# Performance work log

Measured on AMD Instinct MI355X. Metric: run time of the kernel, lower is better.

## Reference

```python
import jax, jax.numpy as jnp
import numpy as np

DIM, HEADS, DIM_HEAD = 1024, 16, 64
INNER = HEADS * DIM_HEAD
EPS = 1e-5

def layernorm(x, w, b):
    mu = jnp.mean(x, axis=-1, keepdims=True)
    var = jnp.var(x, axis=-1, keepdims=True)
    return (x - mu) / jnp.sqrt(var + EPS) * w + b

def setup_inputs() -> dict:
    key = jax.random.key(0)
    ks = jax.random.split(key, 8)
    s = lambda d: 1.0 / np.sqrt(d)
    return {
        'x': jax.random.normal(ks[0], (4, 2048, DIM), jnp.float32),
        'media': jax.random.normal(ks[1], (4, 1024, DIM), jnp.float32),
        'ln_w': jnp.ones((DIM,), jnp.float32),
        'ln_b': jnp.zeros((DIM,), jnp.float32),
        'Wq': jax.random.normal(ks[2], (DIM, INNER), jnp.float32) * s(DIM),
        'Wkv': jax.random.normal(ks[3], (DIM, 2 * INNER), jnp.float32) * s(DIM),
        'Wo': jax.random.normal(ks[4], (INNER, DIM), jnp.float32) * s(INNER),
        'attn_gate': jnp.zeros((1,), jnp.float32),
        'ffln_w': jnp.ones((DIM,), jnp.float32),
        'ffln_b': jnp.zeros((DIM,), jnp.float32),
        'W1': jax.random.normal(ks[5], (DIM, 4 * DIM), jnp.float32) * s(DIM),
        'W2': jax.random.normal(ks[6], (4 * DIM, DIM), jnp.float32) * s(4 * DIM),
    }

def reference(x, media, ln_w, ln_b, Wq, Wkv, Wo, attn_gate, ffln_w, ffln_b, W1, W2):
    scale = DIM_HEAD ** (-0.5)
    b, n, _ = x.shape
    m = media.shape[1]
    # MaskedCrossAttention
    xn = layernorm(x, ln_w, ln_b)
    q = (xn @ Wq).reshape(b, n, HEADS, DIM_HEAD).transpose(0, 2, 1, 3)  # b h n d
    kv = media @ Wkv
    k, v = jnp.split(kv, 2, axis=-1)
    k = k.reshape(b, m, HEADS, DIM_HEAD).transpose(0, 2, 1, 3)  # b h m d
    v = v.reshape(b, m, HEADS, DIM_HEAD).transpose(0, 2, 1, 3)
    sim = jnp.einsum('bhid,bhjd->bhij', q * scale, k)
    # original subtracts detached row-max then softmax: identical to stable softmax
    attn = jax.nn.softmax(sim, axis=-1)
    out = jnp.einsum('bhij,bhjd->bhid', attn, v)
    out = out.transpose(0, 2, 1, 3).reshape(b, n, INNER) @ Wo
    x = out * jnp.tanh(attn_gate) + x
    # FeedForward (note: ff_gate exists in module but is unused in forward)
    h = layernorm(x, ffln_w, ffln_b) @ W1
    h = jax.nn.gelu(h, approximate=False) @ W2
    return h + x
```

## Files before the change

kernel.cpp:

```cpp
#include <hip/hip_runtime.h>
#include <hip/hip_bf16.h>

using bf16 = __hip_bfloat16;
typedef __attribute__((ext_vector_type(8))) short short8;
typedef __attribute__((ext_vector_type(4))) float f32x4;

typedef const void __attribute__((address_space(1))) gvoid;
typedef void __attribute__((address_space(3))) svoid;

__device__ __forceinline__ f32x4 mfma16(short8 a, short8 b, f32x4 c) {
    return __builtin_amdgcn_mfma_f32_16x16x32_bf16(a, b, c, 0, 0, 0);
}

__device__ __forceinline__ void async16(void* lds, const void* g) {
    __builtin_amdgcn_global_load_lds((gvoid*)g, (svoid*)lds, 16, 0, 0);
}

__device__ __forceinline__ unsigned short f2b(float f) {
    bf16 h = __float2bfloat16(f);
    unsigned short u;
    __builtin_memcpy(&u, &h, 2);
    return u;
}

__device__ __forceinline__ float fast_gelu(float x) {
    const float z0 = fmaf(x * x * x, 0.1029432f, 2.3022083f * x);
    const float z = fminf(z0, 80.0f);
    const float e = __builtin_amdgcn_exp2f(z);
    return x * e / (1.0f + e);
}

__global__ __launch_bounds__(256) void prep(
    const float* __restrict__ Wq, const float* __restrict__ Wkv,
    const float* __restrict__ Wo, const float* __restrict__ W1,
    const float* __restrict__ W2, bf16* __restrict__ WqT, bf16* __restrict__ WkvT,
    bf16* __restrict__ WoT, bf16* __restrict__ W1T, bf16* __restrict__ W2T,
    const float* __restrict__ media, bf16* __restrict__ mediab,
    const float* __restrict__ gate, float* __restrict__ gatet) {
    int id = blockIdx.x;
    const float* in;
    bf16* outp;
    int K, N, bx, by;
    if (id < 1024) {
        in = Wq; outp = WqT; K = 1024; N = 1024; bx = id & 31; by = id >> 5;
    } else if (id < 3072) {
        id -= 1024; in = Wkv; outp = WkvT; K = 1024; N = 2048; bx = id & 63; by = id >> 6;
    } else if (id < 4096) {
        id -= 3072; in = Wo; outp = WoT; K = 1024; N = 1024; bx = id & 31; by = id >> 5;
    } else if (id < 8192) {
        id -= 4096; in = W1; outp = W1T; K = 1024; N = 4096; bx = id & 127; by = id >> 7;
    } else if (id < 12288) {
        id -= 8192; in = W2; outp = W2T; K = 4096; N = 1024; bx = id & 31; by = id >> 5;
    } else {
        if (blockIdx.x == 12288 && threadIdx.x == 0) gatet[0] = tanhf(gate[0]);
        id -= 12288;
        const size_t i = (size_t)id * 256 + threadIdx.x;
        float4 v = ((const float4*)media)[i];
        ushort4 o;
        o.x = f2b(v.x); o.y = f2b(v.y); o.z = f2b(v.z); o.w = f2b(v.w);
        ((ushort4*)mediab)[i] = o;
        return;
    }
    __shared__ float tile[32][33];
    const int tx = threadIdx.x & 31, ty = threadIdx.x >> 5;
    const int n0 = bx * 32, k0 = by * 32;
#pragma unroll
    for (int j = 0; j < 32; j += 8)
        tile[ty + j][tx] = in[(size_t)(k0 + ty + j) * N + n0 + tx];
    __syncthreads();
#pragma unroll
    for (int j = 0; j < 32; j += 8)
        outp[(size_t)(n0 + ty + j) * K + k0 + tx] = __float2bfloat16(tile[tx][ty + j]);
}

__global__ __launch_bounds__(256) void layernorm_bf16(
    const float* __restrict__ x, const float* __restrict__ w,
    const float* __restrict__ b, bf16* __restrict__ out) {
    const int row = blockIdx.x, t = threadIdx.x;
    const float4 v = ((const float4*)(x + (size_t)row * 1024))[t];
    float s = v.x + v.y + v.z + v.w;
    float s2 = v.x * v.x + v.y * v.y + v.z * v.z + v.w * v.w;
#pragma unroll
    for (int off = 1; off < 64; off <<= 1) {
        s += __shfl_xor(s, off);
        s2 += __shfl_xor(s2, off);
    }
    __shared__ float rs[4], rs2[4];
    if ((t & 63) == 0) { rs[t >> 6] = s; rs2[t >> 6] = s2; }
    __syncthreads();
    const float S = rs[0] + rs[1] + rs[2] + rs[3];
    const float S2 = rs2[0] + rs2[1] + rs2[2] + rs2[3];
    const float mean = S * (1.0f / 1024.0f);
    const float var = S2 * (1.0f / 1024.0f) - mean * mean;
    const float rstd = rsqrtf(var + 1e-5f);
    const float4 wv = ((const float4*)w)[t];
    const float4 bv = ((const float4*)b)[t];
    ushort4 o;
    o.x = f2b((v.x - mean) * rstd * wv.x + bv.x);
    o.y = f2b((v.y - mean) * rstd * wv.y + bv.y);
    o.z = f2b((v.z - mean) * rstd * wv.z + bv.z);
    o.w = f2b((v.w - mean) * rstd * wv.w + bv.w);
    ((ushort4*)(out + (size_t)row * 1024))[t] = o;
}

__global__ __launch_bounds__(256) void vtranspose(
    const bf16* __restrict__ kvb, bf16* __restrict__ vtg) {
    const int mt = blockIdx.x, bh = blockIdx.y;
    const int b = bh >> 4, h = bh & 15;
    const int m0 = mt * 64;
    __shared__ bf16 tile[64 * 72];
    const int t = threadIdx.x;
#pragma unroll
    for (int i = 0; i < 2; ++i) {
        const int m = i * 32 + (t >> 3);
        short8 v = *(const short8*)(kvb + ((size_t)b * 1024 + m0 + m) * 2048 + 1024 +
                                    (size_t)h * 64 + (t & 7) * 8);
        *(short8*)&tile[m * 72 + (t & 7) * 8] = v;
    }
    __syncthreads();
#pragma unroll
    for (int i = 0; i < 2; ++i) {
        const int d = i * 32 + (t >> 3);
        const int mb = (t & 7) * 8;
        bf16 tmp[8];
#pragma unroll
        for (int j = 0; j < 8; ++j) tmp[j] = tile[(mb + j) * 72 + d];
        *(short8*)(vtg + (size_t)bh * 65536 + (size_t)d * 1024 + m0 + mb) = *(short8*)tmp;
    }
}

enum { EPI_BF16 = 0, EPI_GELU = 1, EPI_GATE_RES = 2, EPI_RES = 3 };

template <int EPI>
__global__ __launch_bounds__(256) void gemm_bf16(
    const bf16* __restrict__ A, const bf16* __restrict__ BT, void* __restrict__ Cout,
    const float* __restrict__ res, const float* __restrict__ gate_p,
    int M, int N, int K) {
    __shared__ bf16 As[2][128 * 64];
    __shared__ bf16 Bs[2][128 * 64];
    const int t = threadIdx.x;
    const int lane = t & 63;
    const int quad = lane >> 4, l15 = lane & 15;
    const int wave = t >> 6;
    const int wm = (wave >> 1) * 64, wn = (wave & 1) * 64;
    const int bm = blockIdx.x * 128, bn = blockIdx.y * 128;

    const int sr = t >> 3;
    const int sc = (t & 7) ^ (sr & 7);
    const bf16* Ag = A + (size_t)(bm + sr) * K + sc * 8;
    const bf16* Bg = BT + (size_t)(bn + sr) * K + sc * 8;

    f32x4 acc[4][4] = {};

    auto stage = [&](int buf, int k0) {
#pragma unroll
        for (int i = 0; i < 4; ++i) {
            async16(&As[buf][i * 2048 + t * 8], Ag + (size_t)i * 32 * K + k0);
            async16(&Bs[buf][i * 2048 + t * 8], Bg + (size_t)i * 32 * K + k0);
        }
    };
    auto compute = [&](int buf) {
#pragma unroll
        for (int dk = 0; dk < 2; ++dk) {
            short8 af[4], bfr[4];
#pragma unroll
            for (int i = 0; i < 4; ++i)
                af[i] = *(const short8*)&As[buf][(wm + i * 16 + l15) * 64 +
                                                 (((dk * 4 + quad) ^ (l15 & 7)) * 8)];
#pragma unroll
            for (int i = 0; i < 4; ++i)
                bfr[i] = *(const short8*)&Bs[buf][(wn + i * 16 + l15) * 64 +
                                                  (((dk * 4 + quad) ^ (l15 & 7)) * 8)];
#pragma unroll
            for (int i = 0; i < 4; ++i)
#pragma unroll
                for (int j = 0; j < 4; ++j)
                    acc[i][j] = mfma16(af[i], bfr[j], acc[i][j]);
        }
    };

    stage(0, 0);
    int cur = 0;
    for (int k0 = 64; k0 < K; k0 += 64) {
        __syncthreads();
        stage(cur ^ 1, k0);
        compute(cur);
        cur ^= 1;
    }
    __syncthreads();
    compute(cur);

    const float gate = (EPI == EPI_GATE_RES) ? gate_p[0] : 0.0f;
#pragma unroll
    for (int i = 0; i < 4; ++i) {
#pragma unroll
        for (int j = 0; j < 4; ++j) {
#pragma unroll
            for (int r = 0; r < 4; ++r) {
                const int row = bm + wm + i * 16 + quad * 4 + r;
                const int col = bn + wn + j * 16 + l15;
                const size_t idx = (size_t)row * N + col;
                const float v = acc[i][j][r];
                if constexpr (EPI == EPI_BF16) {
                    ((bf16*)Cout)[idx] = __float2bfloat16(v);
                } else if constexpr (EPI == EPI_GELU) {
                    ((bf16*)Cout)[idx] = __float2bfloat16(fast_gelu(v));
                } else if constexpr (EPI == EPI_GATE_RES) {
                    ((float*)Cout)[idx] = gate * v + res[idx];
                } else {
                    ((float*)Cout)[idx] = v + res[idx];
                }
            }
        }
    }
}

__global__ __launch_bounds__(256) void attention(
    const bf16* __restrict__ q, const bf16* __restrict__ kvb,
    const bf16* __restrict__ vtg, bf16* __restrict__ out) {
    const int bh = blockIdx.y;
    const int b = bh >> 4, h = bh & 15;
    const int t = threadIdx.x;
    const int wave = t >> 6, lane = t & 63;
    const int quad = lane >> 4, l15 = lane & 15;
    const int qrow0 = blockIdx.x * 128 + wave * 32;

    __shared__ bf16 Ks[2][128 * 64];
    __shared__ bf16 Vts[2][64 * 128];
    __shared__ bf16 Ps[4][16 * 128];

    short8 qa[2][2];
    const size_t qbase = ((size_t)b * 2048 + qrow0) * 1024 + (size_t)h * 64;
#pragma unroll
    for (int g = 0; g < 2; ++g)
#pragma unroll
        for (int dk = 0; dk < 2; ++dk)
            qa[g][dk] = *(const short8*)(q + qbase + (size_t)(g * 16 + l15) * 1024 + dk * 32 + quad * 8);

    f32x4 o[2][4] = {};
    float lsum[2][4] = {};

    const int km = t >> 3;
    const int kc = (t & 7) ^ (km & 7);
    const bf16* ksrc = kvb + ((size_t)b * 1024 + km) * 2048 + (size_t)h * 64 + kc * 8;
    const int vd = t >> 4;
    const int vc = (t & 15) ^ vd;
    const bf16* vsrc = vtg + (size_t)bh * 65536 + (size_t)vd * 1024 + vc * 8;

    bf16* Pw = &Ps[wave][0];

    auto stage = [&](int buf, int m0) {
#pragma unroll
        for (int i = 0; i < 4; ++i) {
            async16(&Ks[buf][i * 2048 + t * 8], ksrc + ((size_t)m0 + i * 32) * 2048);
            async16(&Vts[buf][i * 2048 + t * 8], vsrc + (size_t)i * 16 * 1024 + m0);
        }
    };

    stage(0, 0);
    for (int mc = 0; mc < 8; ++mc) {
        const int cur = mc & 1;
        __syncthreads();
        if (mc < 7) stage(cur ^ 1, (mc + 1) * 128);

#pragma unroll
        for (int g = 0; g < 2; ++g) {
#pragma unroll
            for (int mt = 0; mt < 8; ++mt) {
                f32x4 s = {};
#pragma unroll
                for (int dk = 0; dk < 2; ++dk) {
                    short8 kb = *(const short8*)&Ks[cur][(mt * 16 + l15) * 64 +
                                                    (((dk * 4 + quad) ^ (l15 & 7)) * 8)];
                    s = mfma16(qa[g][dk], kb, s);
                }
                const int pc = mt * 2 + (l15 >> 3);
                const int pj = l15 & 7;
#pragma unroll
                for (int r = 0; r < 4; ++r) {
                    const int row = quad * 4 + r;
                    const float p = __builtin_amdgcn_exp2f(
                        fmaf(s[r], 0.18033688f, -11.5415603f));
                    lsum[g][r] += p;
                    Pw[row * 128 + ((pc ^ row) & 15) * 8 + pj] = __float2bfloat16(p);
                }
            }
            asm volatile("s_waitcnt lgkmcnt(0)" ::: "memory");

#pragma unroll
            for (int ks = 0; ks < 4; ++ks) {
                short8 pa = *(const short8*)&Pw[l15 * 128 + (((ks * 4 + quad) ^ l15) & 15) * 8];
#pragma unroll
                for (int nt = 0; nt < 4; ++nt) {
                    short8 vb = *(const short8*)&Vts[cur][(nt * 16 + l15) * 128 +
                                                     (((ks * 4 + quad) ^ l15) & 15) * 8];
                    o[g][nt] = mfma16(pa, vb, o[g][nt]);
                }
            }
            asm volatile("s_waitcnt lgkmcnt(0)" ::: "memory");
        }
    }

#pragma unroll
    for (int g = 0; g < 2; ++g)
#pragma unroll
        for (int r = 0; r < 4; ++r) {
            float ls = lsum[g][r];
#pragma unroll
            for (int d = 1; d < 16; d <<= 1) ls += __shfl_xor(ls, d);
            lsum[g][r] = 1.0f / ls;
        }

#pragma unroll
    for (int g = 0; g < 2; ++g)
#pragma unroll
        for (int nt = 0; nt < 4; ++nt)
#pragma unroll
            for (int r = 0; r < 4; ++r)
                out[((size_t)b * 2048 + qrow0 + g * 16 + quad * 4 + r) * 1024 +
                    (size_t)h * 64 + nt * 16 + l15] =
                    __float2bfloat16(o[g][nt][r] * lsum[g][r]);
}


extern "C" void kernel_launch(void* const* d_in, const int* in_sizes, int n_in,
                              void* d_out, int out_size, void* d_ws, size_t ws_size,
                              hipStream_t stream) {
    const float* x    = (const float*)d_in[0];
    const float* media= (const float*)d_in[1];
    const float* ln_w = (const float*)d_in[2];
    const float* ln_b = (const float*)d_in[3];
    const float* Wq   = (const float*)d_in[4];
    const float* Wkv  = (const float*)d_in[5];
    const float* Wo   = (const float*)d_in[6];
    const float* gate = (const float*)d_in[7];
    const float* ffw  = (const float*)d_in[8];
    const float* ffb  = (const float*)d_in[9];
    const float* W1   = (const float*)d_in[10];
    const float* W2   = (const float*)d_in[11];
    float* out = (float*)d_out;

    char* p = (char*)d_ws;
    bf16* WqT    = (bf16*)p;               p += (size_t)1024 * 1024 * 2;
    bf16* WkvT   = (bf16*)p;               p += (size_t)2048 * 1024 * 2;
    bf16* WoT    = (bf16*)p;               p += (size_t)1024 * 1024 * 2;
    bf16* W1T    = (bf16*)p;               p += (size_t)4096 * 1024 * 2;
    bf16* W2T    = (bf16*)p;               p += (size_t)1024 * 4096 * 2;
    bf16* xn     = (bf16*)p;               p += (size_t)8192 * 1024 * 2;
    bf16* mediab = (bf16*)p;               p += (size_t)4096 * 1024 * 2;
    bf16* qb     = (bf16*)p;               p += (size_t)8192 * 1024 * 2;
    bf16* kvb    = (bf16*)p;               p += (size_t)4096 * 2048 * 2;
    bf16* vtg    = (bf16*)p;               p += (size_t)64 * 64 * 1024 * 2;
    bf16* attnb  = (bf16*)p;               p += (size_t)8192 * 1024 * 2;
    bf16* hb     = (bf16*)p;               p += (size_t)8192 * 4096 * 2;
    float* x2    = (float*)p;              p += (size_t)8192 * 1024 * 4;
    float* gatet = (float*)p;              p += 256;
    bf16* x2n = xn;

    prep<<<16384, 256, 0, stream>>>(Wq, Wkv, Wo, W1, W2, WqT, WkvT, WoT, W1T, W2T,
                                    media, mediab, gate, gatet);

    layernorm_bf16<<<8192, 256, 0, stream>>>(x, ln_w, ln_b, xn);
    gemm_bf16<EPI_BF16><<<dim3(64, 8), 256, 0, stream>>>(xn, WqT, qb, nullptr, nullptr, 8192, 1024, 1024);
    gemm_bf16<EPI_BF16><<<dim3(32, 16), 256, 0, stream>>>(mediab, WkvT, kvb, nullptr, nullptr, 4096, 2048, 1024);
    vtranspose<<<dim3(16, 64), 256, 0, stream>>>(kvb, vtg);
    attention<<<dim3(16, 64), 256, 0, stream>>>(qb, kvb, vtg, attnb);
    gemm_bf16<EPI_GATE_RES><<<dim3(64, 8), 256, 0, stream>>>(attnb, WoT, x2, x, gatet, 8192, 1024, 1024);

    layernorm_bf16<<<8192, 256, 0, stream>>>(x2, ffw, ffb, x2n);
    gemm_bf16<EPI_GELU><<<dim3(64, 32), 256, 0, stream>>>(x2n, W1T, hb, nullptr, nullptr, 8192, 4096, 1024);
    gemm_bf16<EPI_RES><<<dim3(64, 8), 256, 0, stream>>>(hb, W2T, out, x2, nullptr, 8192, 1024, 4096);
}
```

Before: 492.7 us.

## Add 256x256-tile 8-wave GEMM with interleaved async loads for the W1 GELU GEMM

Adds a new GEMM kernel using 256x256 output tiles, 512 threads and double-buffered LDS filled by async global-to-LDS loads. Those loads are interleaved in four phases with MFMA groups, with barriers and setprio to overlap memory and compute. It is used only for the FFN up-projection (8192x4096x1024) with GELU epilogue, aiming at more data reuse per tile and better latency hiding. The cost is 128KB of LDS per block and heavy register use for 32 accumulators, which limits occupancy, plus fewer blocks (512) across the CUs.

```diff
diff --git a/kernel.cpp b/kernel.cpp
--- a/kernel.cpp
+++ b/kernel.cpp
@@ -215,6 +215,164 @@
     }
 }
 
+template <int EPI>
+__global__ __launch_bounds__(512, 2) void gemm256_bf16(
+    const bf16* __restrict__ A, const bf16* __restrict__ BT, void* __restrict__ Cout,
+    const float* __restrict__ res, const float* __restrict__ gate_p,
+    int M, int N, int K) {
+    __shared__ bf16 As[2][256 * 64];
+    __shared__ bf16 Bs[2][256 * 64];
+    const int t = threadIdx.x;
+    const int lane = t & 63;
+    const int quad = lane >> 4, l15 = lane & 15;
+    const int wave = t >> 6;
+    const int wm = (wave >> 2) * 128;
+    const int wn = (wave & 3) * 64;
+    const int bm = blockIdx.x * 256, bn = blockIdx.y * 256;
+
+    const int sr = t >> 3;
+    const int sc = (t & 7) ^ (sr & 7);
+    const bf16* Ag = A + (size_t)(bm + sr) * K + sc * 8;
+    const bf16* Bg = BT + (size_t)(bn + sr) * K + sc * 8;
+
+    f32x4 acc[8][4] = {};
+
+    auto stA = [&](int buf, int k0, int i) {
+        async16(&As[buf][i * 4096 + t * 8], Ag + (size_t)i * 64 * K + k0);
+    };
+    auto stB = [&](int buf, int k0, int i) {
+        async16(&Bs[buf][i * 4096 + t * 8], Bg + (size_t)i * 64 * K + k0);
+    };
+
+    stB(0, 0, 0); stB(0, 0, 1); stB(0, 0, 2); stB(0, 0, 3);
+    stA(0, 0, 0); stA(0, 0, 2); stA(0, 0, 1); stA(0, 0, 3);
+    asm volatile("s_waitcnt vmcnt(2)" ::: "memory");
+    __builtin_amdgcn_s_barrier();
+    __builtin_amdgcn_sched_barrier(0);
+
+    const int NT = K >> 6;
+    for (int tt = 0; tt < NT; ++tt) {
+        const int cur = tt & 1, nxt = cur ^ 1;
+        const int kn = (tt + 1) << 6;
+        const bool st = (tt + 1 < NT);
+        short8 Af[4][2], Bf[4][2];
+
+#pragma unroll
+        for (int mi = 0; mi < 4; ++mi)
+#pragma unroll
+            for (int ks = 0; ks < 2; ++ks)
+                Af[mi][ks] = *(const short8*)&As[cur][(wm + mi * 16 + l15) * 64 +
+                                                     (((ks * 4 + quad) ^ (l15 & 7)) * 8)];
+#pragma unroll
+        for (int ni = 0; ni < 2; ++ni)
+#pragma unroll
+            for (int ks = 0; ks < 2; ++ks)
+                Bf[ni][ks] = *(const short8*)&Bs[cur][(wn + ni * 16 + l15) * 64 +
+                                                     (((ks * 4 + quad) ^ (l15 & 7)) * 8)];
+        if (st) { stB(nxt, kn, 0); stB(nxt, kn, 1); }
+        asm volatile("s_waitcnt lgkmcnt(8)" ::: "memory");
+        __builtin_amdgcn_s_barrier();
+        asm volatile("s_waitcnt lgkmcnt(0)" ::: "memory");
+        __builtin_amdgcn_sched_barrier(0);
+        __builtin_amdgcn_s_setprio(1);
+#pragma unroll
+        for (int ks = 0; ks < 2; ++ks)
+#pragma unroll
+            for (int mi = 0; mi < 4; ++mi)
+#pragma unroll
+                for (int ni = 0; ni < 2; ++ni)
+                    acc[mi][ni] = mfma16(Af[mi][ks], Bf[ni][ks], acc[mi][ni]);
+        __builtin_amdgcn_s_setprio(0);
+        __builtin_amdgcn_s_barrier();
+        __builtin_amdgcn_sched_barrier(0);
+
+#pragma unroll
+        for (int ni = 2; ni < 4; ++ni)
+#pragma unroll
+            for (int ks = 0; ks < 2; ++ks)
+                Bf[ni][ks] = *(const short8*)&Bs[cur][(wn + ni * 16 + l15) * 64 +
+                                                     (((ks * 4 + quad) ^ (l15 & 7)) * 8)];
+        if (st) { stB(nxt, kn, 2); stB(nxt, kn, 3); }
+        __builtin_amdgcn_s_barrier();
+        asm volatile("s_waitcnt lgkmcnt(0)" ::: "memory");
+        __builtin_amdgcn_sched_barrier(0);
+        __builtin_amdgcn_s_setprio(1);
+#pragma unroll
+        for (int ks = 0; ks < 2; ++ks)
+#pragma unroll
+            for (int mi = 0; mi < 4; ++mi)
+#pragma unroll
+                for (int ni = 2; ni < 4; ++ni)
+                    acc[mi][ni] = mfma16(Af[mi][ks], Bf[ni][ks], acc[mi][ni]);
+        __builtin_amdgcn_s_setprio(0);
+        if (st) asm volatile("s_waitcnt vmcnt(4)" ::: "memory");
+        else    asm volatile("s_waitcnt vmcnt(0)" ::: "memory");
+        __builtin_amdgcn_s_barrier();
+        __builtin_amdgcn_sched_barrier(0);
+
+#pragma unroll
+        for (int mi = 0; mi < 4; ++mi)
+#pragma unroll
+            for (int ks = 0; ks < 2; ++ks)
+                Af[mi][ks] = *(const short8*)&As[cur][(wm + 64 + mi * 16 + l15) * 64 +
+                                                     (((ks * 4 + quad) ^ (l15 & 7)) * 8)];
+        if (st) { stA(nxt, kn, 0); stA(nxt, kn, 2); }
+        __builtin_amdgcn_s_barrier();
+        asm volatile("s_waitcnt lgkmcnt(0)" ::: "memory");
+        __builtin_amdgcn_sched_barrier(0);
+        __builtin_amdgcn_s_setprio(1);
+#pragma unroll
+        for (int ks = 0; ks < 2; ++ks)
+#pragma unroll
+            for (int mi = 0; mi < 4; ++mi)
+#pragma unroll
+                for (int ni = 0; ni < 2; ++ni)
+                    acc[4 + mi][ni] = mfma16(Af[mi][ks], Bf[ni][ks], acc[4 + mi][ni]);
+        __builtin_amdgcn_s_setprio(0);
+        __builtin_amdgcn_s_barrier();
+        __builtin_amdgcn_sched_barrier(0);
+
+        if (st) { stA(nxt, kn, 1); stA(nxt, kn, 3); }
+        __builtin_amdgcn_s_barrier();
+        __builtin_amdgcn_s_setprio(1);
+#pragma unroll
+        for (int ks = 0; ks < 2; ++ks)
+#pragma unroll
+            for (int mi = 0; mi < 4; ++mi)
+#pragma unroll
+                for (int ni = 2; ni < 4; ++ni)
+                    acc[4 + mi][ni] = mfma16(Af[mi][ks], Bf[ni][ks], acc[4 + mi][ni]);
+        __builtin_amdgcn_s_setprio(0);
+        if (st) asm volatile("s_waitcnt vmcnt(2)" ::: "memory");
+        __builtin_amdgcn_s_barrier();
+        __builtin_amdgcn_sched_barrier(0);
+    }
+
+    const float gate = (EPI == EPI_GATE_RES) ? gate_p[0] : 0.0f;
+#pragma unroll
+    for (int mi = 0; mi < 8; ++mi) {
+#pragma unroll
+        for (int ni = 0; ni < 4; ++ni) {
+#pragma unroll
+            for (int r = 0; r < 4; ++r) {
+                const int row = bm + wm + mi * 16 + quad * 4 + r;
+                const int col = bn + wn + ni * 16 + l15;
+                const size_t idx = (size_t)row * N + col;
+                const float v = acc[mi][ni][r];
+                if constexpr (EPI == EPI_BF16) {
+                    ((bf16*)Cout)[idx] = __float2bfloat16(v);
+                } else if constexpr (EPI == EPI_GELU) {
+                    ((bf16*)Cout)[idx] = __float2bfloat16(fast_gelu(v));
+                } else if constexpr (EPI == EPI_GATE_RES) {
+                    ((float*)Cout)[idx] = gate * v + res[idx];
+                } else {
+                    ((float*)Cout)[idx] = v + res[idx];
+                }
+            }
+        }
+    }
+}
+
 __global__ __launch_bounds__(256) void attention(
     const bf16* __restrict__ q, const bf16* __restrict__ kvb,
     const bf16* __restrict__ vtg, bf16* __restrict__ out) {
@@ -368,6 +526,6 @@
     gemm_bf16<EPI_GATE_RES><<<dim3(64, 8), 256, 0, stream>>>(attnb, WoT, x2, x, gatet, 8192, 1024, 1024);
 
     layernorm_bf16<<<8192, 256, 0, stream>>>(x2, ffw, ffb, x2n);
-    gemm_bf16<EPI_GELU><<<dim3(64, 32), 256, 0, stream>>>(x2n, W1T, hb, nullptr, nullptr, 8192, 4096, 1024);
+    gemm256_bf16<EPI_GELU><<<dim3(32, 16), 512, 0, stream>>>(x2n, W1T, hb, nullptr, nullptr, 8192, 4096, 1024);
     gemm_bf16<EPI_RES><<<dim3(64, 8), 256, 0, stream>>>(hb, W2T, out, x2, nullptr, 8192, 1024, 4096);
 }
```

New measurement: 481.7 us. -2.2%, faster.
